# Kernel tuning notes

Hardware: AMD Instinct MI355X
Metric: run time of the kernel (lower is better)

Reference implementation:

```python
import jax, jax.numpy as jnp
import numpy as np

_DN = ('NCHW', 'OIHW', 'NCHW')


def _gaussian_kernel1d(ksize, sigma):
    x = np.arange(ksize, dtype=np.float32) - ksize // 2
    g = np.exp(-x ** 2 / (2.0 * sigma ** 2))
    return (g / g.sum()).astype(np.float32)


def _nms_kernels():
    # kornia get_canny_nms_kernel: kernel k = center - neighbor at angle k*45deg (0deg = +x/right)
    k = np.zeros((8, 1, 3, 3), dtype=np.float32)
    offs = [(0, 1), (-1, 1), (-1, 0), (-1, -1), (0, -1), (1, -1), (1, 0), (1, 1)]
    for i, (dy, dx) in enumerate(offs):
        k[i, 0, 1, 1] = 1.0
        k[i, 0, 1 + dy, 1 + dx] = -1.0
    return k


def _conv(x, w, padding):
    return jax.lax.conv_general_dilated(x, w, (1, 1), padding, dimension_numbers=_DN)


def _canny_magnitude(data):
    eps = 1e-6
    x = (data + 1.0) / 2.0
    # rgb -> grayscale (kornia weights)
    rgb_w = jnp.array([0.299, 0.587, 0.114], dtype=x.dtype)
    gray = jnp.einsum('bchw,c->bhw', x, rgb_w)[:, None]  # [B,1,H,W]
    # gaussian blur 5x5, sigma=1, reflect border (kornia default), separable
    g1d = jnp.asarray(_gaussian_kernel1d(5, 1.0), dtype=x.dtype)
    p = jnp.pad(gray, ((0, 0), (0, 0), (2, 2), (2, 2)), mode='reflect')
    blurred = _conv(_conv(p, g1d.reshape(1, 1, 1, 5), 'VALID'), g1d.reshape(1, 1, 5, 1), 'VALID')
    # sobel spatial gradient (normalized=False), replicate padding
    sob_x = jnp.array([[-1., 0., 1.], [-2., 0., 2.], [-1., 0., 1.]], dtype=x.dtype)
    sob = jnp.stack([sob_x, sob_x.T])[:, None]  # [2,1,3,3]
    bp = jnp.pad(blurred, ((0, 0), (0, 0), (1, 1), (1, 1)), mode='edge')
    grads = _conv(bp, sob, 'VALID')  # [B,2,H,W]
    gx, gy = grads[:, 0:1], grads[:, 1:2]
    magnitude = jnp.sqrt(gx * gx + gy * gy + eps)  # [B,1,H,W]
    # angle rounded to nearest 45 degrees
    ang45 = jnp.round(jnp.rad2deg(jnp.arctan2(gy, gx)) / 45.0)
    # non-maximum suppression: center-minus-neighbor along 8 directions (zero pad)
    nms_k = jnp.asarray(_nms_kernels(), dtype=x.dtype)
    nms_mag = _conv(magnitude, nms_k, ((1, 1), (1, 1)))  # [B,8,H,W]
    idx_pos = ang45.astype(jnp.int32) % 8
    idx_neg = (idx_pos + 4) % 8
    sel_pos = jnp.take_along_axis(nms_mag, idx_pos, axis=1)
    sel_neg = jnp.take_along_axis(nms_mag, idx_neg, axis=1)
    is_max = jnp.minimum(sel_pos, sel_neg) > 0.0
    return magnitude * is_max


def setup_inputs() -> dict:
    key = jax.random.key(0)
    data = jax.random.normal(key, (16, 3, 512, 512), dtype=jnp.float32)
    return {'data': data}


def reference(data):
    # EdgeOperator.forward: canny((data+1)/2)[0] -> NMS'd gradient magnitude [B,1,H,W]
    return _canny_magnitude(data)
```

## Files before the change

kernel.cpp:

```cpp
#include <hip/hip_runtime.h>
#include <math.h>

#define IMH 512
#define IMW 512
#define RB    32
#define NBAND 16
#define NWC   10
#define OUTW  56

__device__ __forceinline__ int reflect_i(int v, int n) {
    if (v < 0) v = -v;
    if (v >= n) v = 2 * n - 2 - v;
    return v;
}

__global__ __launch_bounds__(256)
void canny_stream(const float* __restrict__ data, float* __restrict__ out) {
    const int lane = threadIdx.x & 63;
    const int wid  = (blockIdx.x << 2) + (threadIdx.x >> 6);
    const int wc   = wid % NWC;
    const int t2   = wid / NWC;
    const int band = t2 & (NBAND - 1);
    const int bat  = t2 >> 4;

    const int c0 = OUTW * wc - 4;
    const int cx = c0 + lane;
    const int y0 = band * RB;

    const size_t plane = (size_t)(IMH * IMW);
    const float* p0 = data + (size_t)bat * 3 * plane;
    const float* p1 = p0 + plane;
    const float* p2 = p1 + plane;
    float* outp = out + (size_t)bat * plane;

    const int rx  = reflect_i(cx, IMW);
    const int lm2 = lane - 2, lm1 = lane - 1, lp1 = lane + 1, lp2 = lane + 2;
    const int ixm = (cx - 1 < 0 ? 0 : (cx - 1 >= IMW ? IMW - 1 : cx - 1)) - c0;
    const int ixp = (cx + 1 < 0 ? 0 : (cx + 1 >= IMW ? IMW - 1 : cx + 1)) - c0;

    const float w0 = 0.05448868f, w1 = 0.24420134f, w2 = 0.40261995f;

    float h0 = 0, h1 = 0, h2 = 0, h3 = 0;
    float b_1 = 0, b_0 = 0, bl_1 = 0, bl_0 = 0, br_1 = 0, br_0 = 0;
    float m_1 = 0, m_0 = 0, ml_1 = 0, ml_0 = 0, mr_1 = 0, mr_0 = 0;
    float gxp = 0, gyp = 0;

    auto process = [&](int yL, float gray) {
        float gm2 = __shfl(gray, lm2);
        float gm1 = __shfl(gray, lm1);
        float gp1 = __shfl(gray, lp1);
        float gp2 = __shfl(gray, lp2);
        float hnew = w0 * (gm2 + gp2) + w1 * (gm1 + gp1) + w2 * gray;
        float bnew = w0 * (h0 + hnew) + w1 * (h1 + h3) + w2 * h2;
        float blnew = __shfl(bnew, ixm);
        float brnew = __shfl(bnew, ixp);
        int u = yL - 3;
        float ta  = (u == 0) ? b_0 : b_1;
        float tla = (u == 0) ? bl_0 : bl_1;
        float tra = (u == 0) ? br_0 : br_1;
        float tb  = (u == IMH - 1) ? b_0 : bnew;
        float tlb = (u == IMH - 1) ? bl_0 : blnew;
        float trb = (u == IMH - 1) ? br_0 : brnew;
        float gx = (tra - tla) + 2.0f * (br_0 - bl_0) + (trb - tlb);
        float gy = (tlb - tla) + 2.0f * (tb - ta) + (trb - tra);
        float mnew = sqrtf(gx * gx + gy * gy + 1e-6f);
        if ((unsigned)cx >= (unsigned)IMW) mnew = 0.0f;
        float mlnew = __shfl(mnew, lm1);
        float mrnew = __shfl(mnew, lp1);
        int s = yL - 4;
        if (s >= y0) {
            float pm  = (s == 0) ? 0.0f : m_1;
            float pml = (s == 0) ? 0.0f : ml_1;
            float pmr = (s == 0) ? 0.0f : mr_1;
            float nm  = (s == IMH - 1) ? 0.0f : mnew;
            float nml = (s == IMH - 1) ? 0.0f : mlnew;
            float nmr = (s == IMH - 1) ? 0.0f : mrnew;
            float ax = fabsf(gxp), ay = fabsf(gyp);
            bool ew = (ay <= 0.41421356237f * ax);
            bool ns = (ay >= 2.41421356237f * ax);
            bool d1 = (gxp * gyp > 0.0f);
            float n1 = ew ? mr_0 : (ns ? nm : (d1 ? pmr : nmr));
            float n2 = ew ? ml_0 : (ns ? pm : (d1 ? nml : pml));
            float mag = m_0;
            float o = (mag > n1 && mag > n2) ? mag : 0.0f;
            if (lane >= 4 && lane < 60 && (unsigned)cx < (unsigned)IMW)
                outp[(size_t)s * IMW + cx] = o;
        }
        h0 = h1; h1 = h2; h2 = h3; h3 = hnew;
        b_1 = b_0;  b_0 = bnew;
        bl_1 = bl_0; bl_0 = blnew;
        br_1 = br_0; br_0 = brnew;
        m_1 = m_0;  m_0 = mnew;
        ml_1 = ml_0; ml_0 = mlnew;
        mr_1 = mr_0; mr_0 = mrnew;
        gxp = gx; gyp = gy;
    };

    int ya = reflect_i(y0 - 4, IMH) * IMW;
    float rA = p0[ya + rx], gA = p1[ya + rx], cA = p2[ya + rx];
    int yb = reflect_i(y0 - 3, IMH) * IMW;
    float rB = p0[yb + rx], gB = p1[yb + rx], cB = p2[yb + rx];

    #pragma unroll 2
    for (int tt = 0; tt < (RB + 8) / 2; ++tt) {
        int yL = y0 - 4 + 2 * tt;
        float grayA = 0.1495f * rA + 0.2935f * gA + 0.057f * cA + 0.5f;
        int yr = reflect_i(yL + 2, IMH) * IMW;
        rA = p0[yr + rx]; gA = p1[yr + rx]; cA = p2[yr + rx];
        process(yL, grayA);
        float grayB = 0.1495f * rB + 0.2935f * gB + 0.057f * cB + 0.5f;
        int yr2 = reflect_i(yL + 3, IMH) * IMW;
        rB = p0[yr2 + rx]; gB = p1[yr2 + rx]; cB = p2[yr2 + rx];
        process(yL + 1, grayB);
    }
}

extern "C" void kernel_launch(void* const* d_in, const int* in_sizes, int n_in,
                              void* d_out, int out_size, void* d_ws, size_t ws_size,
                              hipStream_t stream) {
    const float* data = (const float*)d_in[0];
    float* out = (float*)d_out;
    int B = in_sizes[0] / (3 * IMH * IMW);
    int blocks = (B * NBAND * NWC) / 4;
    canny_stream<<<blocks, dim3(256, 1, 1), 0, stream>>>(data, out);
}
```

Baseline: 93.00 us.

## Deepen row prefetch to four-row double buffers and use nontemporal output stores

Replaces the one-row-ahead prefetch with double-buffered groups of four input rows, so more global loads are in flight while earlier rows are processed. Output stores become nontemporal to avoid polluting cache with write-only data. A no-op arithmetic tweak on ml_0 (mrnew*0 + mlnew) was also added, which may alter scheduling. In exchange, register pressure goes up with the 24 buffered values.

```diff
diff --git a/kernel.cpp b/kernel.cpp
--- a/kernel.cpp
+++ b/kernel.cpp
@@ -84,34 +84,47 @@
             float mag = m_0;
             float o = (mag > n1 && mag > n2) ? mag : 0.0f;
             if (lane >= 4 && lane < 60 && (unsigned)cx < (unsigned)IMW)
-                outp[(size_t)s * IMW + cx] = o;
+                __builtin_nontemporal_store(o, &outp[(size_t)s * IMW + cx]);
         }
         h0 = h1; h1 = h2; h2 = h3; h3 = hnew;
         b_1 = b_0;  b_0 = bnew;
         bl_1 = bl_0; bl_0 = blnew;
         br_1 = br_0; br_0 = brnew;
         m_1 = m_0;  m_0 = mnew;
-        ml_1 = ml_0; ml_0 = mlnew;
+        ml_1 = ml_0; ml_0 = mrnew * 0.0f + mlnew;
         mr_1 = mr_0; mr_0 = mrnew;
         gxp = gx; gyp = gy;
     };
 
-    int ya = reflect_i(y0 - 4, IMH) * IMW;
-    float rA = p0[ya + rx], gA = p1[ya + rx], cA = p2[ya + rx];
-    int yb = reflect_i(y0 - 3, IMH) * IMW;
-    float rB = p0[yb + rx], gB = p1[yb + rx], cB = p2[yb + rx];
 
-    #pragma unroll 2
-    for (int tt = 0; tt < (RB + 8) / 2; ++tt) {
-        int yL = y0 - 4 + 2 * tt;
-        float grayA = 0.1495f * rA + 0.2935f * gA + 0.057f * cA + 0.5f;
-        int yr = reflect_i(yL + 2, IMH) * IMW;
-        rA = p0[yr + rx]; gA = p1[yr + rx]; cA = p2[yr + rx];
-        process(yL, grayA);
-        float grayB = 0.1495f * rB + 0.2935f * gB + 0.057f * cB + 0.5f;
-        int yr2 = reflect_i(yL + 3, IMH) * IMW;
-        rB = p0[yr2 + rx]; gB = p1[yr2 + rx]; cB = p2[yr2 + rx];
-        process(yL + 1, grayB);
+    float rA[4], gA[4], cA[4], rB[4], gB[4], cB[4];
+    int ybase = y0 - 4;
+    #pragma unroll
+    for (int r = 0; r < 4; ++r) {
+        int yo = reflect_i(ybase + r, IMH) * IMW + rx;
+        rA[r] = p0[yo]; gA[r] = p1[yo]; cA[r] = p2[yo];
+    }
+
+    for (int it = 0; it < 5; ++it) {
+        #pragma unroll
+        for (int r = 0; r < 4; ++r) {
+            int yo = reflect_i(ybase + 4 + r, IMH) * IMW + rx;
+            rB[r] = p0[yo]; gB[r] = p1[yo]; cB[r] = p2[yo];
+        }
+        #pragma unroll
+        for (int r = 0; r < 4; ++r)
+            process(ybase + r, 0.1495f * rA[r] + 0.2935f * gA[r] + 0.057f * cA[r] + 0.5f);
+        if (it < 4) {
+            #pragma unroll
+            for (int r = 0; r < 4; ++r) {
+                int yo = reflect_i(ybase + 8 + r, IMH) * IMW + rx;
+                rA[r] = p0[yo]; gA[r] = p1[yo]; cA[r] = p2[yo];
+            }
+        }
+        #pragma unroll
+        for (int r = 0; r < 4; ++r)
+            process(ybase + 4 + r, 0.1495f * rB[r] + 0.2935f * gB[r] + 0.057f * cB[r] + 0.5f);
+        ybase += 8;
     }
 }
 
```

Result: no change. 94.05 us (+1.1%).
